# Performance work log

Hardware: AMD Instinct MI355X
Metric: run time of the kernel (lower is better)

The kernel has to match this reference:

```python
import jax, jax.numpy as jnp
import numpy as np

D_MODEL = 768
D_HEAD = 64
BATCH = 2
SEQ = 4096


def setup_inputs() -> dict:
    key = jax.random.key(0)
    k1, k2, k3, k4, k5 = jax.random.split(key, 5)
    x = jax.random.normal(k1, (BATCH, SEQ, D_MODEL), dtype=jnp.float32)
    # causal mask as the module expects: (seq_len, seq_len) float, 1 where attend allowed
    mask = jnp.tril(jnp.ones((SEQ, SEQ), dtype=jnp.float32))
    # weights initialized like the module: randn / sqrt(d_model)
    scale = 1.0 / np.sqrt(D_MODEL)
    Wq = jax.random.normal(k2, (D_HEAD, D_MODEL), dtype=jnp.float32) * scale
    Wk = jax.random.normal(k3, (D_HEAD, D_MODEL), dtype=jnp.float32) * scale
    Wv = jax.random.normal(k4, (D_HEAD, D_MODEL), dtype=jnp.float32) * scale
    Wo = jax.random.normal(k5, (D_MODEL, D_HEAD), dtype=jnp.float32) * scale
    return {"x": x, "mask": mask, "Wq": Wq, "Wk": Wk, "Wv": Wv, "Wo": Wo}


def reference(x, mask, Wq, Wk, Wv, Wo):
    # q,k,v: (B, S, d_head); Linear with weight (out,in) => x @ W.T
    q = jnp.einsum('bsm,hm->bsh', x, Wq)
    k = jnp.einsum('bsm,hm->bsh', x, Wk)
    v = jnp.einsum('bsm,hm->bsh', x, Wv)
    scores = jnp.einsum('bqd,bkd->bqk', q, k) / np.sqrt(D_HEAD)  # (B,S,S)
    seq_len = x.shape[1]
    m = mask[:seq_len, :seq_len]
    # faithful to the torch code: tril(scores) - 1e10 * (1 - mask)
    scores = jnp.tril(scores) - 1e10 * (1.0 - m)
    attn = jax.nn.softmax(scores, axis=-1)
    z = jnp.einsum('bqk,bkd->bqd', attn, v)  # (B,S,d_head)
    out = jnp.einsum('bsh,mh->bsm', z, Wo)   # (B,S,d_model)
    return out
```

## Files before the change

kernel.cpp:

```cpp
#include <hip/hip_runtime.h>
#include <stdint.h>

#define SEQ 4096
#define DM 768
#define DH 64

typedef __attribute__((ext_vector_type(8))) short short8;
typedef __attribute__((ext_vector_type(4))) short short4v;
typedef __attribute__((ext_vector_type(4))) float f32x4;
typedef __attribute__((ext_vector_type(2))) uint32_t uint2v;

#define LOG2E 1.4426950408889634f

static __device__ __forceinline__ short bf16r(float f) {
  union { float f; uint32_t u; } v; v.f = f;
  uint32_t u = v.u;
  return (short)((u + 0x7FFFu + ((u >> 16) & 1u)) >> 16);
}

static __device__ __forceinline__ float bf16f(uint16_t u) {
  union { uint32_t u; float f; } v; v.u = ((uint32_t)u) << 16;
  return v.f;
}

static __device__ __forceinline__ uint32_t cvtpk(float a, float b) {
  uint32_t r;
  asm("v_cvt_pk_bf16_f32 %0, %1, %2" : "=v"(r) : "v"(a), "v"(b));
  return r;
}

static __device__ __forceinline__ int swz(int row, int b) {
  return row * 128 + (b ^ ((row & 7) << 4));
}

static __device__ __forceinline__ void glds16(const void* g, void* l) {
  __builtin_amdgcn_global_load_lds(
      (const __attribute__((address_space(1))) uint32_t*)g,
      (__attribute__((address_space(3))) uint32_t*)l, 16, 0, 0);
}

__global__ __launch_bounds__(256) void convert_w(
    const float* __restrict__ Wq, const float* __restrict__ Wk,
    const float* __restrict__ Wv, const float* __restrict__ Wo,
    uint16_t* __restrict__ Wbp, uint16_t* __restrict__ Wob) {
  int id = blockIdx.x * 256 + threadIdx.x;
  if (id < 18432) {
    int nh = id / 9216, rem = id % 9216;
    int t = rem / 768, rem2 = rem % 768;
    int r = rem2 >> 3, g = rem2 & 7;
    int row = nh * 96 + r;
    const float* src = (row < 64) ? (Wq + (size_t)row * DM)
                     : (row < 128) ? (Wk + (size_t)(row - 64) * DM)
                                   : (Wv + (size_t)(row - 128) * DM);
    const float sc = (row < 64) ? (0.125f * LOG2E) : 1.0f;
    float4 v0 = *(const float4*)(src + t * 64 + g * 8);
    float4 v1 = *(const float4*)(src + t * 64 + g * 8 + 4);
    union { uint32_t u[4]; short8 s; } pk;
    pk.u[0] = cvtpk(v0.x * sc, v0.y * sc);
    pk.u[1] = cvtpk(v0.z * sc, v0.w * sc);
    pk.u[2] = cvtpk(v1.x * sc, v1.y * sc);
    pk.u[3] = cvtpk(v1.z * sc, v1.w * sc);
    char* dst = (char*)Wbp + (size_t)nh * 147456 + t * 12288 + swz(r, g * 16);
    *(short8*)dst = pk.s;
  } else if (id < 30720) {
    int tt = id - 18432;
    int row = tt >> 4, c4 = tt & 15;
    float4 v = *(const float4*)(Wo + (size_t)row * DH + c4 * 4);
    short4v pk = { bf16r(v.x), bf16r(v.y), bf16r(v.z), bf16r(v.w) };
    *(short4v*)(Wob + (size_t)row * DH + c4 * 4) = pk;
  }
}

__global__ __launch_bounds__(256) void qkv_proj(
    const float* __restrict__ x, const uint16_t* __restrict__ Wbp,
    uint16_t* __restrict__ qg, uint16_t* __restrict__ kg, uint16_t* __restrict__ vg) {
  __shared__ char smem[32768] __attribute__((aligned(16)));
  const int tid = threadIdx.x;
  const int lane = tid & 63, wv = tid >> 6;
  const int l15 = lane & 15, l4 = lane >> 4;
  const int row0 = blockIdx.x * 32;
  const int nh = blockIdx.y;
  const char* wsrc = (const char*)Wbp + (size_t)nh * 147456;

  const int xr = tid >> 4, xc4 = tid & 15;
  const int mh = wv & 1, ng = wv >> 1;

  f32x4 acc[3];
  #pragma unroll
  for (int j = 0; j < 3; ++j) acc[j] = (f32x4){0.f, 0.f, 0.f, 0.f};

  float4 xreg[2];
  #pragma unroll
  for (int i = 0; i < 3; ++i)
    glds16(wsrc + wv * 3072 + i * 1024 + lane * 16,
           smem + 8192 + wv * 3072 + i * 1024);
  xreg[0] = *(const float4*)(x + (size_t)(row0 + xr) * DM + xc4 * 4);
  xreg[1] = *(const float4*)(x + (size_t)(row0 + 16 + xr) * DM + xc4 * 4);
  {
    uint2v p0 = { cvtpk(xreg[0].x, xreg[0].y), cvtpk(xreg[0].z, xreg[0].w) };
    *(uint2v*)(smem + swz(xr, xc4 * 8)) = p0;
    uint2v p1 = { cvtpk(xreg[1].x, xreg[1].y), cvtpk(xreg[1].z, xreg[1].w) };
    *(uint2v*)(smem + swz(xr + 16, xc4 * 8)) = p1;
  }

  for (int t = 0; t < 12; ++t) {
    __syncthreads();
    const int buf = t & 1;
    if (t < 11) {
      #pragma unroll
      for (int i = 0; i < 3; ++i)
        glds16(wsrc + (t + 1) * 12288 + wv * 3072 + i * 1024 + lane * 16,
               smem + 8192 + (buf ^ 1) * 12288 + wv * 3072 + i * 1024);
      const int k0n = (t + 1) * 64;
      xreg[0] = *(const float4*)(x + (size_t)(row0 + xr) * DM + k0n + xc4 * 4);
      xreg[1] = *(const float4*)(x + (size_t)(row0 + 16 + xr) * DM + k0n + xc4 * 4);
    }
    {
      char* Xl = smem + buf * 4096;
      char* Wl = smem + 8192 + buf * 12288;
      #pragma unroll
      for (int kc = 0; kc < 2; ++kc) {
        short8 af = *(const short8*)(Xl + swz(mh * 16 + l15, kc * 64 + l4 * 16));
        #pragma unroll
        for (int j = 0; j < 3; ++j) {
          int tl = ng * 3 + j;
          short8 bfv = *(const short8*)(Wl + swz(tl * 16 + l15, kc * 64 + l4 * 16));
          acc[j] = __builtin_amdgcn_mfma_f32_16x16x32_bf16(af, bfv, acc[j], 0, 0, 0);
        }
      }
    }
    if (t < 11) {
      char* Xn = smem + (buf ^ 1) * 4096;
      uint2v p0 = { cvtpk(xreg[0].x, xreg[0].y), cvtpk(xreg[0].z, xreg[0].w) };
      *(uint2v*)(Xn + swz(xr, xc4 * 8)) = p0;
      uint2v p1 = { cvtpk(xreg[1].x, xreg[1].y), cvtpk(xreg[1].z, xreg[1].w) };
      *(uint2v*)(Xn + swz(xr + 16, xc4 * 8)) = p1;
    }
  }
  #pragma unroll
  for (int j = 0; j < 3; ++j) {
    int NT = nh * 6 + ng * 3 + j;
    uint16_t* dst = (NT < 4) ? qg : (NT < 8) ? kg : vg;
    int cb = (NT & 3) * 16 + l15;
    #pragma unroll
    for (int r = 0; r < 4; ++r) {
      int row = row0 + mh * 16 + l4 * 4 + r;
      dst[(size_t)row * DH + cb] = (uint16_t)bf16r(acc[j][r]);
    }
  }
}

__global__ __launch_bounds__(256) void attn_split(
    const uint16_t* __restrict__ qg, const uint16_t* __restrict__ kg,
    const uint16_t* __restrict__ vg, uint16_t* __restrict__ zg,
    uint16_t* __restrict__ Opart, float* __restrict__ Ml, int CHUNK, int MAXCH) {
  __shared__ char smem[32768 + 4 * 2048] __attribute__((aligned(16)));

  const int tid = threadIdx.x;
  const int lane = tid & 63, wv = tid >> 6;
  const int l15 = lane & 15, l4 = lane >> 4;
  const int qt = blockIdx.x, ch = blockIdx.y, b = blockIdx.z;
  const int q0 = qt << 6;
  const int kv_lim = q0 + 64;
  const int kv_begin = ch * CHUNK;
  if (kv_begin >= kv_lim) return;
  const int kv_end = min(kv_begin + CHUNK, kv_lim);
  const int ntiles = (kv_end - kv_begin) >> 6;

  const uint16_t* qb = qg + (size_t)b * SEQ * DH;
  const uint16_t* kb = kg + (size_t)b * SEQ * DH;
  const uint16_t* vb = vg + (size_t)b * SEQ * DH;

  const int qrow = q0 + wv * 16 + l15;
  short8 qf0 = *(const short8*)(qb + (size_t)qrow * DH + l4 * 8);
  short8 qf1 = *(const short8*)(qb + (size_t)qrow * DH + 32 + l4 * 8);

  int koffA[4], koffB[4], voffA[4], voffB[4];
  #pragma unroll
  for (int n = 0; n < 4; ++n) {
    koffA[n] = swz(n * 16 + l15, l4 * 16);
    koffB[n] = swz(n * 16 + l15, 64 + l4 * 16);
    int dr = n * 16 + l15;
    voffA[n] = 8192 + dr * 128 + ((l4 * 16) ^ ((dr & 7) << 4));
    voffB[n] = 8192 + dr * 128 + ((64 + l4 * 16) ^ ((dr & 7) << 4));
  }
  int pwoff[4];
  #pragma unroll
  for (int n = 0; n < 4; ++n) pwoff[n] = 32768 + wv * 2048 + swz(l15, n * 32 + l4 * 8);
  const int proff0 = 32768 + wv * 2048 + swz(l15, l4 * 16);
  const int proff1 = 32768 + wv * 2048 + swz(l15, 64 + l4 * 16);

  const int ku = tid - 128;
  const int vg_ = tid >> 3, vdg = tid & 7;
  short8 sreg[4];
  int soff[8];
  if (tid >= 128) {
    #pragma unroll
    for (int i = 0; i < 4; ++i) {
      int c = ku + (i << 7);
      soff[i] = swz(c >> 3, (c & 7) * 16);
    }
  } else {
    #pragma unroll
    for (int j = 0; j < 8; ++j) {
      int d = vdg * 8 + j;
      soff[j] = 8192 + d * 128 + ((vg_ * 8) ^ ((d & 7) << 4));
    }
  }

#define LOAD_REGS(KV0)                                                              \
  if (tid >= 128) {                                                                 \
    _Pragma("unroll")                                                               \
    for (int i = 0; i < 4; ++i) {                                                   \
      int c = ku + (i << 7);                                                        \
      sreg[i] = *(const short8*)(kb + (size_t)((KV0) + (c >> 3)) * DH + (c & 7) * 8); \
    }                                                                               \
  } else {                                                                          \
    _Pragma("unroll")                                                               \
    for (int i = 0; i < 4; ++i)                                                     \
      sreg[i] = *(const short8*)(vb + (size_t)((KV0) + vg_ * 4 + i) * DH + vdg * 8); \
  }

#define STAGE_WRITE(BUF)                                                            \
  {                                                                                 \
    char* base_ = smem + ((BUF) << 14);                                             \
    if (tid >= 128) {                                                               \
      _Pragma("unroll")                                                             \
      for (int i = 0; i < 4; ++i) *(short8*)(base_ + soff[i]) = sreg[i];            \
    } else {                                                                        \
      _Pragma("unroll")                                                             \
      for (int j = 0; j < 8; ++j) {                                                 \
        short4v pk = { sreg[0][j], sreg[1][j], sreg[2][j], sreg[3][j] };            \
        *(short4v*)(base_ + soff[j]) = pk;                                          \
      }                                                                             \
    }                                                                               \
  }

  LOAD_REGS(kv_begin);
  STAGE_WRITE(0);

  f32x4 oaccT[4];
  #pragma unroll
  for (int n = 0; n < 4; ++n) oaccT[n] = (f32x4){0.f, 0.f, 0.f, 0.f};
  float lrun = 0.f;

  for (int T = 0; T < ntiles; ++T) {
    const int kv0 = kv_begin + (T << 6);
    const bool more = (T + 1 < ntiles);
    if (more) { LOAD_REGS(kv0 + 64); }
    __syncthreads();
    char* cb_ = smem + ((T & 1) << 14);

    f32x4 sacc[4];
    #pragma unroll
    for (int n = 0; n < 4; ++n) sacc[n] = (f32x4){0.f, 0.f, 0.f, 0.f};
    __builtin_amdgcn_s_setprio(1);
    #pragma unroll
    for (int n = 0; n < 4; ++n) {
      short8 kf0 = *(const short8*)(cb_ + koffA[n]);
      sacc[n] = __builtin_amdgcn_mfma_f32_16x16x32_bf16(kf0, qf0, sacc[n], 0, 0, 0);
      short8 kf1 = *(const short8*)(cb_ + koffB[n]);
      sacc[n] = __builtin_amdgcn_mfma_f32_16x16x32_bf16(kf1, qf1, sacc[n], 0, 0, 0);
    }
    __builtin_amdgcn_s_setprio(0);

    if (more) { STAGE_WRITE((T + 1) & 1); }

    if (kv0 + 63 > q0) {
      #pragma unroll
      for (int n = 0; n < 4; ++n) {
        #pragma unroll
        for (int r = 0; r < 4; ++r) {
          int kvg = kv0 + n * 16 + l4 * 4 + r;
          if (kvg > qrow) sacc[n][r] = -1e30f;
        }
      }
    }

    float ls = 0.f;
    #pragma unroll
    for (int n = 0; n < 4; ++n) {
      #pragma unroll
      for (int r = 0; r < 4; ++r) {
        float p = __builtin_amdgcn_exp2f(sacc[n][r]);
        sacc[n][r] = p;
        ls += p;
      }
    }
    ls += __shfl_xor(ls, 16);
    ls += __shfl_xor(ls, 32);
    lrun += ls;

    #pragma unroll
    for (int n = 0; n < 4; ++n) {
      uint2v pk = { cvtpk(sacc[n][0], sacc[n][1]), cvtpk(sacc[n][2], sacc[n][3]) };
      *(uint2v*)(smem + pwoff[n]) = pk;
    }
    asm volatile("s_waitcnt lgkmcnt(0)" ::: "memory");
    short8 pa0 = *(const short8*)(smem + proff0);
    short8 pa1 = *(const short8*)(smem + proff1);
    __builtin_amdgcn_s_setprio(1);
    #pragma unroll
    for (int n = 0; n < 4; ++n) {
      short8 vf0 = *(const short8*)(cb_ + voffA[n]);
      oaccT[n] = __builtin_amdgcn_mfma_f32_16x16x32_bf16(vf0, pa0, oaccT[n], 0, 0, 0);
      short8 vf1 = *(const short8*)(cb_ + voffB[n]);
      oaccT[n] = __builtin_amdgcn_mfma_f32_16x16x32_bf16(vf1, pa1, oaccT[n], 0, 0, 0);
    }
    __builtin_amdgcn_s_setprio(0);
  }
#undef LOAD_REGS
#undef STAGE_WRITE

  const int rl = wv * 16 + l15;
  if (MAXCH == 1) {
    float invl = 1.0f / lrun;
    uint16_t* zb = zg + (size_t)b * SEQ * DH;
    #pragma unroll
    for (int n = 0; n < 4; ++n) {
      short4v pk = { bf16r(oaccT[n][0] * invl), bf16r(oaccT[n][1] * invl),
                     bf16r(oaccT[n][2] * invl), bf16r(oaccT[n][3] * invl) };
      *(short4v*)(zb + (size_t)(q0 + rl) * DH + n * 16 + l4 * 4) = pk;
    }
  } else {
    const size_t slot = ((size_t)(b << 6) + qt) * MAXCH + ch;
    uint16_t* op = Opart + slot * 4096;
    #pragma unroll
    for (int n = 0; n < 4; ++n) {
      short4v pk = { bf16r(oaccT[n][0]), bf16r(oaccT[n][1]),
                     bf16r(oaccT[n][2]), bf16r(oaccT[n][3]) };
      *(short4v*)(op + (size_t)rl * 64 + n * 16 + l4 * 4) = pk;
    }
    if (l4 == 0) Ml[slot * 64 + rl] = lrun;
  }
}

__global__ __launch_bounds__(256) void out_proj(
    const uint16_t* __restrict__ Opart, const float* __restrict__ Ml,
    const uint16_t* __restrict__ zg, const uint16_t* __restrict__ Wob,
    float* __restrict__ out, int CHUNK, int MAXCH) {
  __shared__ char smem[4096 + 32768] __attribute__((aligned(16)));
  char* Zl = smem;
  char* Wl = smem + 4096;
  const int tid = threadIdx.x;
  const int lane = tid & 63, wv = tid >> 6;
  const int l15 = lane & 15, l4 = lane >> 4;
  const int row0 = blockIdx.x * 32;
  const int col0 = blockIdx.y * 256;

  {
    const int r = tid >> 3, c0 = (tid & 7) << 3;
    if (MAXCH == 1) {
      short8 v = *(const short8*)(zg + (size_t)(row0 + r) * DH + c0);
      *(short8*)(Zl + swz(r, c0 * 2)) = v;
    } else {
      const int b = row0 >> 12;
      const int rlb = row0 & 4095;
      const int qt = rlb >> 6, q0 = qt << 6;
      const int row_local = (rlb & 63) + r;
      const int nch = (q0 + 64 + CHUNK - 1) / CHUNK;
      const size_t sbase = ((size_t)(b << 6) + qt) * MAXCH;
      float a[8] = {0.f, 0.f, 0.f, 0.f, 0.f, 0.f, 0.f, 0.f};
      float wsum = 0.f;
      for (int ch = 0; ch < nch; ++ch) {
        const size_t s = sbase + ch;
        wsum += Ml[s * 64 + row_local];
        short8 v = *(const short8*)(Opart + s * 4096 + (size_t)row_local * 64 + c0);
        #pragma unroll
        for (int j = 0; j < 8; ++j) a[j] += bf16f((uint16_t)v[j]);
      }
      float inv = 1.0f / wsum;
      short8 pk;
      #pragma unroll
      for (int j = 0; j < 8; ++j) pk[j] = bf16r(a[j] * inv);
      *(short8*)(Zl + swz(r, c0 * 2)) = pk;
    }
  }
  #pragma unroll
  for (int i = 0; i < 8; ++i) {
    int id = tid + (i << 8);
    int m = id >> 3, c8 = id & 7;
    short8 vw = *(const short8*)(Wob + (size_t)(col0 + m) * DH + c8 * 8);
    *(short8*)(Wl + swz(m, c8 * 16)) = vw;
  }
  __syncthreads();

  const int mh = wv & 1, ng = wv >> 1;
  short8 af0 = *(const short8*)(Zl + swz(mh * 16 + l15, l4 * 16));
  short8 af1 = *(const short8*)(Zl + swz(mh * 16 + l15, 64 + l4 * 16));
  f32x4 acc[8];
  #pragma unroll
  for (int j = 0; j < 8; ++j) acc[j] = (f32x4){0.f, 0.f, 0.f, 0.f};
  #pragma unroll
  for (int j = 0; j < 8; ++j) {
    int nt = ng * 8 + j;
    short8 b0 = *(const short8*)(Wl + swz(nt * 16 + l15, l4 * 16));
    acc[j] = __builtin_amdgcn_mfma_f32_16x16x32_bf16(af0, b0, acc[j], 0, 0, 0);
    short8 b1 = *(const short8*)(Wl + swz(nt * 16 + l15, 64 + l4 * 16));
    acc[j] = __builtin_amdgcn_mfma_f32_16x16x32_bf16(af1, b1, acc[j], 0, 0, 0);
  }
  #pragma unroll
  for (int j = 0; j < 8; ++j) {
    int nt = ng * 8 + j;
    #pragma unroll
    for (int r = 0; r < 4; ++r) {
      int row = row0 + mh * 16 + l4 * 4 + r;
      int col = col0 + nt * 16 + l15;
      out[(size_t)row * DM + col] = acc[j][r];
    }
  }
}

extern "C" void kernel_launch(void* const* d_in, const int* in_sizes, int n_in,
                              void* d_out, int out_size, void* d_ws, size_t ws_size,
                              hipStream_t stream) {
  const float* x  = (const float*)d_in[0];
  const float* Wq = (const float*)d_in[2];
  const float* Wk = (const float*)d_in[3];
  const float* Wv = (const float*)d_in[4];
  const float* Wo = (const float*)d_in[5];
  float* out = (float*)d_out;

  const size_t N = (size_t)2 * SEQ * DH;
  uint16_t* qg = (uint16_t*)d_ws;
  uint16_t* kg = qg + N;
  uint16_t* vg = kg + N;
  uint16_t* zg = vg + N;
  uint16_t* Wbp = zg + N;
  const size_t WBE = (size_t)192 * DM;
  uint16_t* Wob = Wbp + WBE;
  const size_t WOE = (size_t)DM * DH;
  uint16_t* Opart = Wob + WOE;

  int maxch = 16;
  while (maxch > 1) {
    size_t slots = (size_t)2 * 64 * maxch;
    size_t need = 4 * N * 2 + WBE * 2 + WOE * 2 + slots * (4096 * 2 + 64 * 4);
    if (need <= ws_size) break;
    maxch >>= 1;
  }
  const int CHUNK = SEQ / maxch;
  float* Ml = (float*)(Opart + (size_t)2 * 64 * maxch * 4096);

  convert_w<<<120, 256, 0, stream>>>(Wq, Wk, Wv, Wo, Wbp, Wob);
  qkv_proj<<<dim3(256, 2), 256, 0, stream>>>(x, Wbp, qg, kg, vg);
  attn_split<<<dim3(64, maxch, 2), 256, 0, stream>>>(qg, kg, vg, zg, Opart, Ml,
                                                     CHUNK, maxch);
  out_proj<<<dim3(256, 3), 256, 0, stream>>>(Opart, Ml, zg, Wob, out, CHUNK, maxch);
}
```

Baseline: 48.91 us.

## Triple-buffer QKV projection with two-stage-ahead prefetch and explicit waitcnt

The QKV projection loop moves from double to triple buffering in shared memory. Loads for the weight and x tiles are now issued two iterations ahead, and __syncthreads is replaced by explicit vmcnt/lgkmcnt waits plus s_barrier, with sched_barriers added. The aim is to hide global-load latency behind the MFMA work. In exchange the block uses 48KB of LDS, which may lower occupancy, and the hand-counted vmcnt values must match the number of loads in flight.

Result: faster. 47.73 us (-2.4%).

```diff
diff --git a/kernel.cpp b/kernel.cpp
--- a/kernel.cpp
+++ b/kernel.cpp
@@ -74,7 +74,7 @@
 __global__ __launch_bounds__(256) void qkv_proj(
     const float* __restrict__ x, const uint16_t* __restrict__ Wbp,
     uint16_t* __restrict__ qg, uint16_t* __restrict__ kg, uint16_t* __restrict__ vg) {
-  __shared__ char smem[32768] __attribute__((aligned(16)));
+  __shared__ char smem[49152] __attribute__((aligned(16)));
   const int tid = threadIdx.x;
   const int lane = tid & 63, wv = tid >> 6;
   const int l15 = lane & 15, l4 = lane >> 4;
@@ -85,39 +85,57 @@
   const int xr = tid >> 4, xc4 = tid & 15;
   const int mh = wv & 1, ng = wv >> 1;
 
+  const float* xp0 = x + (size_t)(row0 + xr) * DM + xc4 * 4;
+  const float* xp1 = x + (size_t)(row0 + 16 + xr) * DM + xc4 * 4;
+
   f32x4 acc[3];
   #pragma unroll
   for (int j = 0; j < 3; ++j) acc[j] = (f32x4){0.f, 0.f, 0.f, 0.f};
 
-  float4 xreg[2];
+  float4 xrg[2][2];
+  xrg[0][0] = *(const float4*)(xp0);
+  xrg[0][1] = *(const float4*)(xp1);
   #pragma unroll
   for (int i = 0; i < 3; ++i)
-    glds16(wsrc + wv * 3072 + i * 1024 + lane * 16,
-           smem + 8192 + wv * 3072 + i * 1024);
-  xreg[0] = *(const float4*)(x + (size_t)(row0 + xr) * DM + xc4 * 4);
-  xreg[1] = *(const float4*)(x + (size_t)(row0 + 16 + xr) * DM + xc4 * 4);
+    glds16(wsrc + i * 1024 + wv * 3072 + lane * 16,
+           smem + 12288 + wv * 3072 + i * 1024);
+  __builtin_amdgcn_sched_barrier(0);
+  xrg[1][0] = *(const float4*)(xp0 + 64);
+  xrg[1][1] = *(const float4*)(xp1 + 64);
+  #pragma unroll
+  for (int i = 0; i < 3; ++i)
+    glds16(wsrc + 12288 + wv * 3072 + i * 1024 + lane * 16,
+           smem + 12288 + 12288 + wv * 3072 + i * 1024);
+  __builtin_amdgcn_sched_barrier(0);
   {
-    uint2v p0 = { cvtpk(xreg[0].x, xreg[0].y), cvtpk(xreg[0].z, xreg[0].w) };
+    uint2v p0 = { cvtpk(xrg[0][0].x, xrg[0][0].y), cvtpk(xrg[0][0].z, xrg[0][0].w) };
     *(uint2v*)(smem + swz(xr, xc4 * 8)) = p0;
-    uint2v p1 = { cvtpk(xreg[1].x, xreg[1].y), cvtpk(xreg[1].z, xreg[1].w) };
+    uint2v p1 = { cvtpk(xrg[0][1].x, xrg[0][1].y), cvtpk(xrg[0][1].z, xrg[0][1].w) };
     *(uint2v*)(smem + swz(xr + 16, xc4 * 8)) = p1;
   }
 
+  #pragma unroll
   for (int t = 0; t < 12; ++t) {
-    __syncthreads();
-    const int buf = t & 1;
+    asm volatile("s_waitcnt lgkmcnt(0)" ::: "memory");
     if (t < 11) {
+      asm volatile("s_waitcnt vmcnt(5)" ::: "memory");
+    } else {
+      asm volatile("s_waitcnt vmcnt(0)" ::: "memory");
+    }
+    __builtin_amdgcn_s_barrier();
+    if (t < 10) {
+      const int k2 = (t + 2) * 64;
+      xrg[t & 1][0] = *(const float4*)(xp0 + k2);
+      xrg[t & 1][1] = *(const float4*)(xp1 + k2);
       #pragma unroll
       for (int i = 0; i < 3; ++i)
-        glds16(wsrc + (t + 1) * 12288 + wv * 3072 + i * 1024 + lane * 16,
-               smem + 8192 + (buf ^ 1) * 12288 + wv * 3072 + i * 1024);
-      const int k0n = (t + 1) * 64;
-      xreg[0] = *(const float4*)(x + (size_t)(row0 + xr) * DM + k0n + xc4 * 4);
-      xreg[1] = *(const float4*)(x + (size_t)(row0 + 16 + xr) * DM + k0n + xc4 * 4);
+        glds16(wsrc + (t + 2) * 12288 + wv * 3072 + i * 1024 + lane * 16,
+               smem + 12288 + ((t + 2) % 3) * 12288 + wv * 3072 + i * 1024);
+      __builtin_amdgcn_sched_barrier(0);
     }
     {
-      char* Xl = smem + buf * 4096;
-      char* Wl = smem + 8192 + buf * 12288;
+      char* Xl = smem + (t % 3) * 4096;
+      char* Wl = smem + 12288 + (t % 3) * 12288;
       #pragma unroll
       for (int kc = 0; kc < 2; ++kc) {
         short8 af = *(const short8*)(Xl + swz(mh * 16 + l15, kc * 64 + l4 * 16));
@@ -130,10 +148,11 @@
       }
     }
     if (t < 11) {
-      char* Xn = smem + (buf ^ 1) * 4096;
-      uint2v p0 = { cvtpk(xreg[0].x, xreg[0].y), cvtpk(xreg[0].z, xreg[0].w) };
+      char* Xn = smem + ((t + 1) % 3) * 4096;
+      float4 a0 = xrg[(t + 1) & 1][0], a1 = xrg[(t + 1) & 1][1];
+      uint2v p0 = { cvtpk(a0.x, a0.y), cvtpk(a0.z, a0.w) };
       *(uint2v*)(Xn + swz(xr, xc4 * 8)) = p0;
-      uint2v p1 = { cvtpk(xreg[1].x, xreg[1].y), cvtpk(xreg[1].z, xreg[1].w) };
+      uint2v p1 = { cvtpk(a1.x, a1.y), cvtpk(a1.z, a1.w) };
       *(uint2v*)(Xn + swz(xr + 16, xc4 * 8)) = p1;
     }
   }
```
